# Kernel optimization log

Hardware: AMD Instinct MI355X
Metric: run time of the kernel (lower is better)

## Reference

```python
import jax, jax.numpy as jnp
import numpy as np

VIS_ENC_DIM = 1024
SENT_HIDDEN_DIM = 512
ATT_DIM = 512
B, L = 64, 1024


def setup_inputs() -> dict:
    key = jax.random.key(0)
    ks = jax.random.split(key, 8)
    s_enc = 1.0 / np.sqrt(VIS_ENC_DIM)
    s_dec = 1.0 / np.sqrt(SENT_HIDDEN_DIM)
    s_full = 1.0 / np.sqrt(ATT_DIM)
    return {
        "vis_enc_output": jax.random.normal(ks[0], (B, L, VIS_ENC_DIM), jnp.float32),
        "dec_hidden_state": jax.random.normal(ks[1], (B, SENT_HIDDEN_DIM), jnp.float32),
        "W_enc": jax.random.uniform(ks[2], (VIS_ENC_DIM, ATT_DIM), jnp.float32, -s_enc, s_enc),
        "b_enc": jax.random.uniform(ks[3], (ATT_DIM,), jnp.float32, -s_enc, s_enc),
        "W_dec": jax.random.uniform(ks[4], (SENT_HIDDEN_DIM, ATT_DIM), jnp.float32, -s_dec, s_dec),
        "b_dec": jax.random.uniform(ks[5], (ATT_DIM,), jnp.float32, -s_dec, s_dec),
        "w_full": jax.random.uniform(ks[6], (ATT_DIM,), jnp.float32, -s_full, s_full),
        "b_full": jax.random.uniform(ks[7], (), jnp.float32, -s_full, s_full),
    }


def reference(vis_enc_output, dec_hidden_state, W_enc, b_enc, W_dec, b_dec, w_full, b_full):
    # enc projection: [B, L, A]
    vis_enc_att = jnp.einsum('blv,va->bla', vis_enc_output, W_enc) + b_enc
    # dec projection: [B, A]
    dec_output = dec_hidden_state @ W_dec + b_dec
    # broadcast add + tanh, then reduce over att dim -> scores [B, L]
    joined = jnp.tanh(vis_enc_att + dec_output[:, None, :])
    logits = jnp.einsum('bla,a->bl', joined, w_full) + b_full
    att_scores = jax.nn.softmax(logits, axis=1)
    # weighted sum over L -> [B, V]
    att_output = jnp.einsum('bl,blv->bv', att_scores, vis_enc_output)
    return att_output, att_scores
```

## Files before the change

kernel.cpp:

```cpp
#include <hip/hip_runtime.h>
#include <hip/hip_bf16.h>
#include <stdint.h>


typedef __attribute__((ext_vector_type(8))) short bf16x8;
typedef __attribute__((ext_vector_type(8))) unsigned short ushortx8;
typedef __attribute__((ext_vector_type(4))) float f32x4;

#define LOG2E 1.4426950408889634f

__device__ __forceinline__ unsigned short f2bf(float f) {
  uint32_t u = __builtin_bit_cast(uint32_t, f);
  u += 0x7FFFu + ((u >> 16) & 1u);
  return (unsigned short)(u >> 16);
}

__device__ __forceinline__ float fast_tanh(float x) {
  float e = __builtin_amdgcn_exp2f(x * 2.885390081777927f);
  return 1.0f - 2.0f * __builtin_amdgcn_rcpf(e + 1.0f);
}

__device__ __forceinline__ void load_lds16(const void* g, void* l) {
  __builtin_amdgcn_global_load_lds(
      (const __attribute__((address_space(1))) void*)g,
      (__attribute__((address_space(3))) void*)l, 16, 0, 0);
}

__global__ __launch_bounds__(256) void k0_pack_w(const float* __restrict__ W,
                                                 unsigned short* __restrict__ Wst) {
  const int S = blockIdx.x * 256 + threadIdx.x;
  const int t = S >> 11;
  const int s = S & 2047;
  const int a = s >> 2;
  const int kb = s & 3;
  const int k0 = t * 32 + kb * 8;
  ushortx8 p;
#pragma unroll
  for (int j = 0; j < 8; ++j) p[j] = f2bf(W[(size_t)(k0 + j) * 512 + a]);
  *(ushortx8*)(Wst + (size_t)S * 8) = p;
}

__global__ __launch_bounds__(256) void k1_dproj(const float* __restrict__ dec,
                                                const float* __restrict__ Wd,
                                                const float* __restrict__ bd,
                                                const float* __restrict__ be,
                                                float* __restrict__ dproj,
                                                float* __restrict__ logits) {
  const int b = blockIdx.x;
  const int tid = threadIdx.x;
#pragma unroll
  for (int j = 0; j < 4; ++j) logits[b * 1024 + j * 256 + tid] = 0.0f;
  float a0 = 0.f, a1 = 0.f;
  const float* dr = dec + b * 512;
  for (int h = 0; h < 512; ++h) {
    float d = dr[h];
    a0 = fmaf(d, Wd[h * 512 + tid], a0);
    a1 = fmaf(d, Wd[h * 512 + tid + 256], a1);
  }
  dproj[b * 512 + tid] = a0 + bd[tid] + be[tid];
  dproj[b * 512 + tid + 256] = a1 + bd[tid + 256] + be[tid + 256];
}

__global__ __launch_bounds__(256, 2) void k2_fused_gemm(
    const float* __restrict__ vis, const unsigned short* __restrict__ Wst,
    const float* __restrict__ dproj, const float* __restrict__ wfull,
    float* __restrict__ logits) {
  alignas(16) __shared__ unsigned short Al[2][2048];
  alignas(16) __shared__ unsigned short Bl[2][16384];

  const int tid = threadIdx.x;
  const int lane = tid & 63;
  const int w = tid >> 6;
  const int blk = blockIdx.x;
  const int b = blk >> 4;
  const size_t mbase = (size_t)blk * 64;

  const int arow = tid >> 2;
  const int akb = tid & 3;
  const float* asrc = vis + (mbase + (size_t)arow) * 1024 + akb * 8;
  const int a_dst = akb * 512 + arow * 8;

  const unsigned short* bsrc = Wst + (size_t)w * 4096 + (size_t)lane * 8;

  f32x4 acc[4][8];
#pragma unroll
  for (int m = 0; m < 4; ++m)
#pragma unroll
    for (int n = 0; n < 8; ++n) acc[m][n] = (f32x4){0.f, 0.f, 0.f, 0.f};

  auto stage = [&](int t, int buf) {
    const unsigned short* bs = bsrc + (size_t)t * 16384;
#pragma unroll
    for (int j = 0; j < 8; ++j)
      load_lds16(bs + j * 512, &Bl[buf][w * 4096 + j * 512]);
    const float* as = asrc + (size_t)t * 32;
    f32x4 x0 = *(const f32x4*)(as);
    f32x4 x1 = *(const f32x4*)(as + 4);
    ushortx8 p;
    p[0] = f2bf(x0[0]); p[1] = f2bf(x0[1]); p[2] = f2bf(x0[2]); p[3] = f2bf(x0[3]);
    p[4] = f2bf(x1[0]); p[5] = f2bf(x1[1]); p[6] = f2bf(x1[2]); p[7] = f2bf(x1[3]);
    *(ushortx8*)(&Al[buf][a_dst]) = p;
  };

  stage(0, 0);

  const int a_rd = (lane >> 4) * 512 + (lane & 15) * 8;
  const int b_rd = w * 4096 + (lane & 15) * 32 + (lane >> 4) * 8;

  for (int t = 0; t < 32; ++t) {
    const int cur = t & 1;
    __syncthreads();
    if (t < 31) stage(t + 1, cur ^ 1);
    bf16x8 af[4];
#pragma unroll
    for (int m = 0; m < 4; ++m) af[m] = *(const bf16x8*)(&Al[cur][a_rd + m * 128]);
    bf16x8 bfr[8];
#pragma unroll
    for (int n = 0; n < 8; ++n) bfr[n] = *(const bf16x8*)(&Bl[cur][b_rd + n * 512]);
#pragma unroll
    for (int m = 0; m < 4; ++m)
#pragma unroll
      for (int n = 0; n < 8; ++n)
        acc[m][n] = __builtin_amdgcn_mfma_f32_16x16x32_bf16(af[m], bfr[n], acc[m][n], 0, 0, 0);
  }

  const float* dp = dproj + b * 512 + w * 128 + (lane & 15);
  const float* wf = wfull + w * 128 + (lane & 15);
  float dpv[8], wfv[8];
#pragma unroll
  for (int n = 0; n < 8; ++n) { dpv[n] = dp[n * 16]; wfv[n] = wf[n * 16]; }

#pragma unroll
  for (int m = 0; m < 4; ++m) {
#pragma unroll
    for (int r = 0; r < 4; ++r) {
      float s = 0.f;
#pragma unroll
      for (int n = 0; n < 8; ++n)
        s += wfv[n] * fast_tanh(acc[m][n][r] + dpv[n]);
      s += __shfl_xor(s, 1, 64);
      s += __shfl_xor(s, 2, 64);
      s += __shfl_xor(s, 4, 64);
      s += __shfl_xor(s, 8, 64);
      if ((lane & 15) == 0) {
        int row = m * 16 + (lane >> 4) * 4 + r;
        atomicAdd(&logits[mbase + row], s);
      }
    }
  }
}

__global__ __launch_bounds__(256) void k3_softmax(const float* __restrict__ logits,
                                                  float* __restrict__ out) {
  const int b = blockIdx.x;
  const int tid = threadIdx.x;
#pragma unroll
  for (int j = 0; j < 4; ++j) out[b * 1024 + j * 256 + tid] = 0.f;

  float x[4];
#pragma unroll
  for (int j = 0; j < 4; ++j) x[j] = logits[b * 1024 + j * 256 + tid];
  float mx = fmaxf(fmaxf(x[0], x[1]), fmaxf(x[2], x[3]));
#pragma unroll
  for (int d = 1; d < 64; d <<= 1) mx = fmaxf(mx, __shfl_xor(mx, d, 64));
  __shared__ float redm[4], reds[4];
  if ((tid & 63) == 0) redm[tid >> 6] = mx;
  __syncthreads();
  mx = fmaxf(fmaxf(redm[0], redm[1]), fmaxf(redm[2], redm[3]));
  float e[4];
  float s = 0.f;
#pragma unroll
  for (int j = 0; j < 4; ++j) {
    e[j] = __builtin_amdgcn_exp2f((x[j] - mx) * LOG2E);
    s += e[j];
  }
#pragma unroll
  for (int d = 1; d < 64; d <<= 1) s += __shfl_xor(s, d, 64);
  if ((tid & 63) == 0) reds[tid >> 6] = s;
  __syncthreads();
  s = reds[0] + reds[1] + reds[2] + reds[3];
  float inv = 1.0f / s;
#pragma unroll
  for (int j = 0; j < 4; ++j) out[65536 + b * 1024 + j * 256 + tid] = e[j] * inv;
}

__global__ __launch_bounds__(256) void k4_attout(const float* __restrict__ vis,
                                                 const float* __restrict__ scores,
                                                 float* __restrict__ out) {
  const int b = blockIdx.x;
  const int chunk = blockIdx.y;
  const int tid = threadIdx.x;
  const float* sc = scores + b * 1024 + chunk * 128;
  const f32x4* vbase = (const f32x4*)(vis + ((size_t)b * 1024 + (size_t)chunk * 128) * 1024) + tid;
  f32x4 acc = (f32x4){0.f, 0.f, 0.f, 0.f};
  for (int l = 0; l < 128; ++l) {
    float s = sc[l];
    f32x4 v = vbase[(size_t)l * 256];
    acc += v * s;
  }
  float* o = out + b * 1024 + tid * 4;
  atomicAdd(o + 0, acc[0]);
  atomicAdd(o + 1, acc[1]);
  atomicAdd(o + 2, acc[2]);
  atomicAdd(o + 3, acc[3]);
}

extern "C" void kernel_launch(void* const* d_in, const int* in_sizes, int n_in,
                              void* d_out, int out_size, void* d_ws, size_t ws_size,
                              hipStream_t stream) {
  const float* vis = (const float*)d_in[0];
  const float* dec = (const float*)d_in[1];
  const float* Wenc = (const float*)d_in[2];
  const float* benc = (const float*)d_in[3];
  const float* Wdec = (const float*)d_in[4];
  const float* bdec = (const float*)d_in[5];
  const float* wfull = (const float*)d_in[6];
  float* out = (float*)d_out;
  char* ws = (char*)d_ws;
  unsigned short* Wst = (unsigned short*)ws;
  float* dproj = (float*)(ws + (1 << 20));
  float* logits = (float*)(ws + (1 << 20) + (128 << 10));

  hipLaunchKernelGGL(k0_pack_w, dim3(256), dim3(256), 0, stream, Wenc, Wst);
  hipLaunchKernelGGL(k1_dproj, dim3(64), dim3(256), 0, stream, dec, Wdec, bdec, benc, dproj, logits);
  hipLaunchKernelGGL(k2_fused_gemm, dim3(1024), dim3(256), 0, stream, vis, Wst, dproj, wfull, logits);
  hipLaunchKernelGGL(k3_softmax, dim3(64), dim3(256), 0, stream, logits, out);
  hipLaunchKernelGGL(k4_attout, dim3(64, 8), dim3(256), 0, stream, vis, out + 65536, out);
}
```

Baseline: 498.3 us.

## Merge prep kernels, enlarge GEMM tile to 128 rows, fuse softmax into attout

Combines the weight-packing and decoder-projection kernels into one launch, with the decoder projection split across more blocks. The attention GEMM tile grows to 128 rows x 512 columns with 8 waves, so each W_enc tile loaded into LDS serves twice as many rows, and vis loads are issued two steps ahead in registers. Softmax is recomputed redundantly inside each attout block, removing a separate launch. The larger tile halves the grid to 512 blocks at one block per CU, which may cut occupancy and latency hiding.

```diff
diff --git a/kernel.cpp b/kernel.cpp
--- a/kernel.cpp
+++ b/kernel.cpp
@@ -26,61 +26,67 @@
       (__attribute__((address_space(3))) void*)l, 16, 0, 0);
 }
 
-__global__ __launch_bounds__(256) void k0_pack_w(const float* __restrict__ W,
-                                                 unsigned short* __restrict__ Wst) {
-  const int S = blockIdx.x * 256 + threadIdx.x;
-  const int t = S >> 11;
-  const int s = S & 2047;
-  const int a = s >> 2;
-  const int kb = s & 3;
-  const int k0 = t * 32 + kb * 8;
-  ushortx8 p;
-#pragma unroll
-  for (int j = 0; j < 8; ++j) p[j] = f2bf(W[(size_t)(k0 + j) * 512 + a]);
-  *(ushortx8*)(Wst + (size_t)S * 8) = p;
-}
-
-__global__ __launch_bounds__(256) void k1_dproj(const float* __restrict__ dec,
+__global__ __launch_bounds__(256) void k01_prep(const float* __restrict__ W,
+                                                unsigned short* __restrict__ Wst,
+                                                const float* __restrict__ dec,
                                                 const float* __restrict__ Wd,
                                                 const float* __restrict__ bd,
                                                 const float* __restrict__ be,
                                                 float* __restrict__ dproj,
-                                                float* __restrict__ logits) {
-  const int b = blockIdx.x;
+                                                float* __restrict__ logits,
+                                                float* __restrict__ out) {
   const int tid = threadIdx.x;
-#pragma unroll
-  for (int j = 0; j < 4; ++j) logits[b * 1024 + j * 256 + tid] = 0.0f;
-  float a0 = 0.f, a1 = 0.f;
-  const float* dr = dec + b * 512;
-  for (int h = 0; h < 512; ++h) {
-    float d = dr[h];
-    a0 = fmaf(d, Wd[h * 512 + tid], a0);
-    a1 = fmaf(d, Wd[h * 512 + tid + 256], a1);
-  }
-  dproj[b * 512 + tid] = a0 + bd[tid] + be[tid];
-  dproj[b * 512 + tid + 256] = a1 + bd[tid + 256] + be[tid + 256];
-}
-
-__global__ __launch_bounds__(256, 2) void k2_fused_gemm(
+  if (blockIdx.x < 256) {
+    const int S = blockIdx.x * 256 + tid;
+    const int t = S >> 11;
+    const int kb = (S >> 9) & 3;
+    const int a = S & 511;
+    const int k0 = t * 32 + kb * 8;
+    ushortx8 p;
+#pragma unroll
+    for (int j = 0; j < 8; ++j) p[j] = f2bf(W[(size_t)(k0 + j) * 512 + a]);
+    *(ushortx8*)(Wst + (size_t)S * 8) = p;
+  } else {
+    const int q = blockIdx.x - 256;
+    logits[q * 256 + tid] = 0.0f;
+    out[q * 256 + tid] = 0.0f;
+    const int b = q >> 2;
+    const int a = (q & 3) * 128 + (tid & 127);
+    const int hh = tid >> 7;
+    const float* dr = dec + b * 512 + hh * 256;
+    const float* wc = Wd + (size_t)(hh * 256) * 512 + a;
+    float acc = 0.f;
+#pragma unroll 8
+    for (int h = 0; h < 256; ++h) acc = fmaf(dr[h], wc[(size_t)h * 512], acc);
+    __shared__ float sh[128];
+    if (hh == 1) sh[tid & 127] = acc;
+    __syncthreads();
+    if (hh == 0) dproj[b * 512 + a] = acc + sh[tid] + bd[a] + be[a];
+  }
+}
+
+__global__ __launch_bounds__(512, 1) void k2_fused_gemm(
     const float* __restrict__ vis, const unsigned short* __restrict__ Wst,
     const float* __restrict__ dproj, const float* __restrict__ wfull,
     float* __restrict__ logits) {
-  alignas(16) __shared__ unsigned short Al[2][2048];
+  alignas(16) __shared__ unsigned short Al[2][4096];
   alignas(16) __shared__ unsigned short Bl[2][16384];
 
   const int tid = threadIdx.x;
   const int lane = tid & 63;
   const int w = tid >> 6;
+  const int wm = w >> 2;
+  const int wn = w & 3;
   const int blk = blockIdx.x;
-  const int b = blk >> 4;
-  const size_t mbase = (size_t)blk * 64;
+  const int b = blk >> 3;
+  const size_t mbase = (size_t)blk * 128;
 
   const int arow = tid >> 2;
   const int akb = tid & 3;
   const float* asrc = vis + (mbase + (size_t)arow) * 1024 + akb * 8;
-  const int a_dst = akb * 512 + arow * 8;
-
-  const unsigned short* bsrc = Wst + (size_t)w * 4096 + (size_t)lane * 8;
+  const int a_dst = akb * 1024 + arow * 8;
+
+  const unsigned short* bsrc = Wst + (size_t)w * 2048 + (size_t)lane * 8;
 
   f32x4 acc[4][8];
 #pragma unroll
@@ -88,44 +94,58 @@
 #pragma unroll
     for (int n = 0; n < 8; ++n) acc[m][n] = (f32x4){0.f, 0.f, 0.f, 0.f};
 
-  auto stage = [&](int t, int buf) {
+  auto bload = [&](int t, int buf) {
     const unsigned short* bs = bsrc + (size_t)t * 16384;
 #pragma unroll
-    for (int j = 0; j < 8; ++j)
-      load_lds16(bs + j * 512, &Bl[buf][w * 4096 + j * 512]);
+    for (int j = 0; j < 4; ++j)
+      load_lds16(bs + j * 512, &Bl[buf][w * 2048 + j * 512]);
+  };
+  auto aload = [&](int t, f32x4* x) {
     const float* as = asrc + (size_t)t * 32;
-    f32x4 x0 = *(const f32x4*)(as);
-    f32x4 x1 = *(const f32x4*)(as + 4);
+    x[0] = *(const f32x4*)(as);
+    x[1] = *(const f32x4*)(as + 4);
+  };
+  auto awrite = [&](int buf, const f32x4* x) {
     ushortx8 p;
-    p[0] = f2bf(x0[0]); p[1] = f2bf(x0[1]); p[2] = f2bf(x0[2]); p[3] = f2bf(x0[3]);
-    p[4] = f2bf(x1[0]); p[5] = f2bf(x1[1]); p[6] = f2bf(x1[2]); p[7] = f2bf(x1[3]);
+    p[0] = f2bf(x[0][0]); p[1] = f2bf(x[0][1]); p[2] = f2bf(x[0][2]); p[3] = f2bf(x[0][3]);
+    p[4] = f2bf(x[1][0]); p[5] = f2bf(x[1][1]); p[6] = f2bf(x[1][2]); p[7] = f2bf(x[1][3]);
     *(ushortx8*)(&Al[buf][a_dst]) = p;
   };
 
-  stage(0, 0);
-
-  const int a_rd = (lane >> 4) * 512 + (lane & 15) * 8;
-  const int b_rd = w * 4096 + (lane & 15) * 32 + (lane >> 4) * 8;
-
-  for (int t = 0; t < 32; ++t) {
-    const int cur = t & 1;
+  const int a_rd = (lane >> 4) * 1024 + (wm * 64 + (lane & 15)) * 8;
+  const int b_rd = (lane >> 4) * 4096 + (wn * 128 + (lane & 15)) * 8;
+
+  f32x4 xA[2], xB[2];
+  bload(0, 0);
+  aload(0, xA);
+  awrite(0, xA);
+  aload(1, xA);
+
+  auto step = [&](int t, int cur, f32x4* xc, f32x4* xn) {
     __syncthreads();
-    if (t < 31) stage(t + 1, cur ^ 1);
+    if (t < 31) bload(t + 1, cur ^ 1);
+    if (t < 30) aload(t + 2, xn);
     bf16x8 af[4];
 #pragma unroll
     for (int m = 0; m < 4; ++m) af[m] = *(const bf16x8*)(&Al[cur][a_rd + m * 128]);
     bf16x8 bfr[8];
 #pragma unroll
-    for (int n = 0; n < 8; ++n) bfr[n] = *(const bf16x8*)(&Bl[cur][b_rd + n * 512]);
+    for (int n = 0; n < 8; ++n) bfr[n] = *(const bf16x8*)(&Bl[cur][b_rd + n * 128]);
 #pragma unroll
     for (int m = 0; m < 4; ++m)
 #pragma unroll
       for (int n = 0; n < 8; ++n)
         acc[m][n] = __builtin_amdgcn_mfma_f32_16x16x32_bf16(af[m], bfr[n], acc[m][n], 0, 0, 0);
-  }
-
-  const float* dp = dproj + b * 512 + w * 128 + (lane & 15);
-  const float* wf = wfull + w * 128 + (lane & 15);
+    if (t < 31) awrite(cur ^ 1, xc);
+  };
+
+  for (int tt = 0; tt < 32; tt += 2) {
+    step(tt, 0, xA, xB);
+    step(tt + 1, 1, xB, xA);
+  }
+
+  const float* dp = dproj + b * 512 + wn * 128 + (lane & 15);
+  const float* wf = wfull + wn * 128 + (lane & 15);
   float dpv[8], wfv[8];
 #pragma unroll
   for (int n = 0; n < 8; ++n) { dpv[n] = dp[n * 16]; wfv[n] = wf[n * 16]; }
@@ -143,61 +163,65 @@
       s += __shfl_xor(s, 4, 64);
       s += __shfl_xor(s, 8, 64);
       if ((lane & 15) == 0) {
-        int row = m * 16 + (lane >> 4) * 4 + r;
+        int row = wm * 64 + m * 16 + (lane >> 4) * 4 + r;
         atomicAdd(&logits[mbase + row], s);
       }
     }
   }
 }
 
-__global__ __launch_bounds__(256) void k3_softmax(const float* __restrict__ logits,
+__global__ __launch_bounds__(256) void k34_attout(const float* __restrict__ logits,
+                                                  const float* __restrict__ vis,
                                                   float* __restrict__ out) {
-  const int b = blockIdx.x;
-  const int tid = threadIdx.x;
-#pragma unroll
-  for (int j = 0; j < 4; ++j) out[b * 1024 + j * 256 + tid] = 0.f;
-
-  float x[4];
-#pragma unroll
-  for (int j = 0; j < 4; ++j) x[j] = logits[b * 1024 + j * 256 + tid];
-  float mx = fmaxf(fmaxf(x[0], x[1]), fmaxf(x[2], x[3]));
-#pragma unroll
-  for (int d = 1; d < 64; d <<= 1) mx = fmaxf(mx, __shfl_xor(mx, d, 64));
-  __shared__ float redm[4], reds[4];
-  if ((tid & 63) == 0) redm[tid >> 6] = mx;
-  __syncthreads();
-  mx = fmaxf(fmaxf(redm[0], redm[1]), fmaxf(redm[2], redm[3]));
-  float e[4];
-  float s = 0.f;
-#pragma unroll
-  for (int j = 0; j < 4; ++j) {
-    e[j] = __builtin_amdgcn_exp2f((x[j] - mx) * LOG2E);
-    s += e[j];
-  }
-#pragma unroll
-  for (int d = 1; d < 64; d <<= 1) s += __shfl_xor(s, d, 64);
-  if ((tid & 63) == 0) reds[tid >> 6] = s;
-  __syncthreads();
-  s = reds[0] + reds[1] + reds[2] + reds[3];
-  float inv = 1.0f / s;
-#pragma unroll
-  for (int j = 0; j < 4; ++j) out[65536 + b * 1024 + j * 256 + tid] = e[j] * inv;
-}
-
-__global__ __launch_bounds__(256) void k4_attout(const float* __restrict__ vis,
-                                                 const float* __restrict__ scores,
-                                                 float* __restrict__ out) {
   const int b = blockIdx.x;
   const int chunk = blockIdx.y;
   const int tid = threadIdx.x;
-  const float* sc = scores + b * 1024 + chunk * 128;
-  const f32x4* vbase = (const f32x4*)(vis + ((size_t)b * 1024 + (size_t)chunk * 128) * 1024) + tid;
-  f32x4 acc = (f32x4){0.f, 0.f, 0.f, 0.f};
-  for (int l = 0; l < 128; ++l) {
-    float s = sc[l];
-    f32x4 v = vbase[(size_t)l * 256];
-    acc += v * s;
-  }
+  const int wid = tid >> 6;
+  const int lane = tid & 63;
+  const float* base = logits + b * 1024;
+
+  float x[4];
+#pragma unroll
+  for (int j = 0; j < 4; ++j) x[j] = base[j * 256 + tid];
+  float mx = fmaxf(fmaxf(x[0], x[1]), fmaxf(x[2], x[3]));
+#pragma unroll
+  for (int d = 1; d < 64; d <<= 1) mx = fmaxf(mx, __shfl_xor(mx, d, 64));
+  __shared__ float redm[4], reds[4];
+  if (lane == 0) redm[wid] = mx;
+  __syncthreads();
+  mx = fmaxf(fmaxf(redm[0], redm[1]), fmaxf(redm[2], redm[3]));
+  float s = 0.f;
+#pragma unroll
+  for (int j = 0; j < 4; ++j) s += __builtin_amdgcn_exp2f((x[j] - mx) * LOG2E);
+#pragma unroll
+  for (int d = 1; d < 64; d <<= 1) s += __shfl_xor(s, d, 64);
+  if (lane == 0) reds[wid] = s;
+  __syncthreads();
+  s = reds[0] + reds[1] + reds[2] + reds[3];
+  const float inv = 1.0f / s;
+
+  if (chunk == 0) {
+#pragma unroll
+    for (int j = 0; j < 4; ++j)
+      out[65536 + b * 1024 + j * 256 + tid] =
+          __builtin_amdgcn_exp2f((x[j] - mx) * LOG2E) * inv;
+  }
+
+  __shared__ float p[128];
+  const int l0 = chunk * 128;
+  if (tid < 128)
+    p[tid] = __builtin_amdgcn_exp2f((base[l0 + tid] - mx) * LOG2E) * inv;
+  __syncthreads();
+
+  const f32x4* vb = (const f32x4*)(vis + ((size_t)b * 1024 + (size_t)l0) * 1024) + tid;
+  f32x4 acc0 = (f32x4){0.f, 0.f, 0.f, 0.f};
+  f32x4 acc1 = (f32x4){0.f, 0.f, 0.f, 0.f};
+#pragma unroll 4
+  for (int l = 0; l < 128; l += 2) {
+    acc0 += vb[(size_t)l * 256] * p[l];
+    acc1 += vb[(size_t)(l + 1) * 256] * p[l + 1];
+  }
+  f32x4 acc = acc0 + acc1;
   float* o = out + b * 1024 + tid * 4;
   atomicAdd(o + 0, acc[0]);
   atomicAdd(o + 1, acc[1]);
@@ -221,9 +245,10 @@
   float* dproj = (float*)(ws + (1 << 20));
   float* logits = (float*)(ws + (1 << 20) + (128 << 10));
 
-  hipLaunchKernelGGL(k0_pack_w, dim3(256), dim3(256), 0, stream, Wenc, Wst);
-  hipLaunchKernelGGL(k1_dproj, dim3(64), dim3(256), 0, stream, dec, Wdec, bdec, benc, dproj, logits);
-  hipLaunchKernelGGL(k2_fused_gemm, dim3(1024), dim3(256), 0, stream, vis, Wst, dproj, wfull, logits);
-  hipLaunchKernelGGL(k3_softmax, dim3(64), dim3(256), 0, stream, logits, out);
-  hipLaunchKernelGGL(k4_attout, dim3(64, 8), dim3(256), 0, stream, vis, out + 65536, out);
-}
+  hipLaunchKernelGGL(k01_prep, dim3(512), dim3(256), 0, stream,
+                     Wenc, Wst, dec, Wdec, bdec, benc, dproj, logits, out);
+  hipLaunchKernelGGL(k2_fused_gemm, dim3(512), dim3(512), 0, stream,
+                     vis, Wst, dproj, wfull, logits);
+  hipLaunchKernelGGL(k34_attout, dim3(64, 8), dim3(256), 0, stream,
+                     logits, vis, out);
+}
```

Result: no change. 489.0 us (-1.9%).
